# Kernel tuning notes

Measured on AMD Instinct MI355X. Metric: run time of the kernel, lower is better.

## Reference

```python
import jax, jax.numpy as jnp
import numpy as np

STATE_LEN = 128
SEQ_LEN = 2048
NUM_ITERS = 2
DIM_IN = 1024
DIM_H = 64
BATCH = 2
T_TOTAL = SEQ_LEN + 2 * STATE_LEN  # 2304
NEG = -1e30  # large-negative causal mask (avoids -inf NaNs under autodiff)


def _ln(x, g, b):
    m = jnp.mean(x, axis=-1, keepdims=True)
    v = jnp.var(x, axis=-1, keepdims=True)
    return (x - m) / jnp.sqrt(v + 1e-5) * g + b


def setup_inputs() -> dict:
    key = jax.random.key(0)
    ks = jax.random.split(key, 16)

    def w(k, fi, fo):
        # torch nn.Linear-style fan-in scaled init (keeps logits O(1))
        return jax.random.normal(k, (fi, fo), jnp.float32) / np.sqrt(fi)

    return {
        "x": jax.random.normal(ks[0], (BATCH, T_TOTAL, DIM_IN), jnp.float32),
        "Wh": w(ks[1], DIM_IN, DIM_H),
        "Whs": w(ks[2], DIM_IN, DIM_H),
        "Whe": w(ks[3], DIM_IN, DIM_H),
        "Wk": w(ks[4], DIM_H, DIM_H),
        "Wq": w(ks[5], DIM_H, DIM_H),
        "Wv": w(ks[6], DIM_H, DIM_H),
        "Wks": w(ks[7], DIM_H, DIM_H),
        "Wqs": w(ks[8], DIM_H, DIM_H),
        "Wvs": w(ks[9], DIM_H, DIM_H),
        "Wke": w(ks[10], DIM_H, DIM_H),
        "Wqe": w(ks[11], DIM_H, DIM_H),
        "Wve": w(ks[12], DIM_H, DIM_H),
        "ln_g": jnp.ones((DIM_IN,), jnp.float32),
        "ln_b": jnp.zeros((DIM_IN,), jnp.float32),
        "ln_gs": jnp.ones((DIM_IN,), jnp.float32),
        "ln_bs": jnp.zeros((DIM_IN,), jnp.float32),
        "ln_ge": jnp.ones((DIM_IN,), jnp.float32),
        "ln_be": jnp.zeros((DIM_IN,), jnp.float32),
        "cope_emb": jax.random.normal(ks[13], (DIM_H, T_TOTAL), jnp.float32),
    }


def reference(x, Wh, Whs, Whe, Wk, Wq, Wv, Wks, Wqs, Wvs, Wke, Wqe, Wve,
              ln_g, ln_b, ln_gs, ln_bs, ln_ge, ln_be, cope_emb):
    S = STATE_LEN
    # extract_state: [state_start | seq | state_end] along token dim
    xs, xm, xe = x[:, :S], x[:, S:-S], x[:, -S:]
    xm = _ln(xm, ln_g, ln_b)
    xs = _ln(xs, ln_gs, ln_bs)
    xe = _ln(xe, ln_ge, ln_be)

    mem = xm @ Wh                 # (B, L, D)
    mem_s = xs @ Whs              # (B, S, D)
    mem_e = xe @ Whe              # (B, S, D)

    scale = 1.0 / np.sqrt(DIM_H)  # xformers default scale (beta=None)
    tril = jnp.tril(jnp.ones((T_TOTAL, T_TOTAL), bool))
    mask = jnp.where(tril, 0.0, NEG)  # log of lower-triangular ones

    mem_full = None
    for ix in range(NUM_ITERS):
        k = jnp.concatenate([mem_s @ Wks, mem @ Wk, mem_e @ Wke], axis=1)  # (B,T,D)
        q = jnp.concatenate([mem_s @ Wqs, mem @ Wq, mem_e @ Wqe], axis=1)
        v = jnp.concatenate([mem_s @ Wvs, mem @ Wv, mem_e @ Wve], axis=1)

        logits = jnp.einsum('btd,bsd->bts', q, k)  # unscaled, as in CoPE gates
        if ix == 0:
            # CoPE: sigmoid-gated reverse cumsum positions + interpolated embedding bias
            gates = jax.nn.sigmoid(logits)
            pos = jnp.flip(jnp.cumsum(jnp.flip(gates, -1), axis=-1), -1)
            pos = jnp.minimum(pos, float(T_TOTAL - 1))
            pos_floor = jnp.floor(pos)
            pos_ceil = jnp.ceil(pos)
            logits_int = jnp.einsum('btd,dn->btn', q, cope_emb)  # (B,T,T)
            lc = jnp.take_along_axis(logits_int, pos_ceil.astype(jnp.int32), axis=-1)
            lf = jnp.take_along_axis(logits_int, pos_floor.astype(jnp.int32), axis=-1)
            wfrac = pos - pos_floor
            bias = lc * wfrac + lf * (1.0 - wfrac)
            scores = logits * scale + mask + bias
        else:
            scores = logits * scale + mask

        attn = jax.nn.softmax(scores, axis=-1)
        mem_full = jnp.einsum('bts,bsd->btd', attn, v)  # (B,T,D)
        if ix < NUM_ITERS - 1:
            mem_s, mem, mem_e = mem_full[:, :S], mem_full[:, S:-S], mem_full[:, -S:]
    return mem_full
```

## Files before the change

### kernel.cpp

```cpp
#include <hip/hip_runtime.h>

#define T_TOT 2304
#define S_LEN 128
#define D_IN  1024
#define D_H   64
#define BATCH 2
#define NROW  (BATCH * T_TOT)
#define CH    (T_TOT / 256)
#define SCALE 0.125f
#define KCHUNKS 8
#define KCW   (D_IN / KCHUNKS)

typedef unsigned short u16;
typedef __attribute__((ext_vector_type(8))) short short8;
typedef __attribute__((ext_vector_type(4))) float f32x4;
typedef __attribute__((ext_vector_type(4))) unsigned short u16x4;

static __device__ __forceinline__ u16 f2bf(float f) {
    unsigned u = __float_as_uint(f);
    unsigned r = (u + 0x7fffu + ((u >> 16) & 1u)) >> 16;
    return (u16)r;
}
static __device__ __forceinline__ float bf2f(u16 s) {
    return __uint_as_float((unsigned)s << 16);
}

__global__ __launch_bounds__(256) void k_ln(
    const float* __restrict__ x,
    const float* __restrict__ ln_g,  const float* __restrict__ ln_b,
    const float* __restrict__ ln_gs, const float* __restrict__ ln_bs,
    const float* __restrict__ ln_ge, const float* __restrict__ ln_be,
    u16* __restrict__ xn_hi, u16* __restrict__ xn_lo)
{
    __shared__ float red1[256], red2[256];
    const int row = blockIdx.x;
    const int t = row % T_TOT;
    const int tid = threadIdx.x;

    const float *gg, *bb;
    if (t < S_LEN)               { gg = ln_gs; bb = ln_bs; }
    else if (t >= T_TOT - S_LEN) { gg = ln_ge; bb = ln_be; }
    else                         { gg = ln_g;  bb = ln_b;  }

    const float4 xv = *(const float4*)(x + (size_t)row * D_IN + 4 * tid);
    float s  = xv.x + xv.y + xv.z + xv.w;
    float s2 = xv.x * xv.x + xv.y * xv.y + xv.z * xv.z + xv.w * xv.w;
    red1[tid] = s; red2[tid] = s2; __syncthreads();
    for (int off = 128; off > 0; off >>= 1) {
        if (tid < off) { red1[tid] += red1[tid + off]; red2[tid] += red2[tid + off]; }
        __syncthreads();
    }
    const float mean = red1[0] * (1.f / D_IN);
    const float var  = red2[0] * (1.f / D_IN) - mean * mean;
    const float rstd = rsqrtf(var + 1e-5f);

    const float4 gv = *(const float4*)(gg + 4 * tid);
    const float4 bv = *(const float4*)(bb + 4 * tid);
    float o0 = (xv.x - mean) * rstd * gv.x + bv.x;
    float o1 = (xv.y - mean) * rstd * gv.y + bv.y;
    float o2 = (xv.z - mean) * rstd * gv.z + bv.z;
    float o3 = (xv.w - mean) * rstd * gv.w + bv.w;

    u16x4 hv, lv;
    hv[0] = f2bf(o0); lv[0] = f2bf(o0 - bf2f(hv[0]));
    hv[1] = f2bf(o1); lv[1] = f2bf(o1 - bf2f(hv[1]));
    hv[2] = f2bf(o2); lv[2] = f2bf(o2 - bf2f(hv[2]));
    hv[3] = f2bf(o3); lv[3] = f2bf(o3 - bf2f(hv[3]));
    *(u16x4*)(xn_hi + (size_t)row * D_IN + 4 * tid) = hv;
    *(u16x4*)(xn_lo + (size_t)row * D_IN + 4 * tid) = lv;
}

#define WPREP_N (3 * D_H * D_IN)
__global__ __launch_bounds__(256) void k_prep(
    const float* __restrict__ Wh, const float* __restrict__ Whs, const float* __restrict__ Whe,
    const float* __restrict__ cope,
    u16* __restrict__ wT_hi, u16* __restrict__ wT_lo,
    u16* __restrict__ cT_hi, u16* __restrict__ cT_lo)
{
    const int gid = blockIdx.x * 256 + threadIdx.x;
    if (gid < WPREP_N) {
        const int seg = gid >> 16;
        const int o = gid & 65535;
        const int j = o >> 10, k = o & 1023;
        const float* W = seg == 0 ? Wh : (seg == 1 ? Whs : Whe);
        const float f = W[k * D_H + j];
        const u16 hi = f2bf(f);
        wT_hi[gid] = hi;
        wT_lo[gid] = f2bf(f - bf2f(hi));
    } else {
        const int idx = gid - WPREP_N;
        if (idx < T_TOT * D_H) {
            const int n = idx >> 6, d = idx & 63;
            const float f = cope[(size_t)d * T_TOT + n];
            const u16 hi = f2bf(f);
            cT_hi[idx] = hi;
            cT_lo[idx] = f2bf(f - bf2f(hi));
        }
    }
}

__global__ __launch_bounds__(256) void k_hgemm(
    const u16* __restrict__ xn_hi, const u16* __restrict__ xn_lo,
    const u16* __restrict__ wT_hi, const u16* __restrict__ wT_lo,
    float* __restrict__ h_part)
{
    const int tile = blockIdx.x;
    const int kc   = blockIdx.y;
    const int k0   = kc * KCW;
    const int tt = tile % 36;
    const int seg = tt < 2 ? 1 : (tt >= 34 ? 2 : 0);

    __shared__ u16 Bh[64 * KCW];
    __shared__ u16 Bl[64 * KCW];

    const int tid = threadIdx.x;
    {
        const int r = tid >> 2;
        const int c0 = (tid & 3) * 32;
        const u16* sh = wT_hi + ((size_t)seg * D_H + r) * D_IN + k0 + c0;
        const u16* sl = wT_lo + ((size_t)seg * D_H + r) * D_IN + k0 + c0;
        const int sw = (r & 7) << 3;
        #pragma unroll
        for (int u = 0; u < 4; ++u) {
            const int col = c0 + 8 * u;
            *(short8*)&Bh[r * KCW + (col ^ sw)] = *(const short8*)(sh + 8 * u);
            *(short8*)&Bl[r * KCW + (col ^ sw)] = *(const short8*)(sl + 8 * u);
        }
    }
    __syncthreads();

    const int w = tid >> 6;
    const int lane = tid & 63;
    const int l15 = lane & 15, lg4 = lane >> 4;
    const int row0 = tile * 64 + w * 16;

    const size_t abase = (size_t)(row0 + l15) * D_IN + k0 + 8 * lg4;
    f32x4 acc[4] = {};

    #pragma unroll
    for (int kk = 0; kk < KCW / 32; ++kk) {
        short8 ah = *(const short8*)(xn_hi + abase + kk * 32);
        short8 al = *(const short8*)(xn_lo + abase + kk * 32);
        #pragma unroll
        for (int j = 0; j < 4; ++j) {
            const int brow = j * 16 + l15;
            const int col = (kk * 32 + 8 * lg4) ^ ((brow & 7) << 3);
            short8 bh = *(const short8*)&Bh[brow * KCW + col];
            short8 bl = *(const short8*)&Bl[brow * KCW + col];
            acc[j] = __builtin_amdgcn_mfma_f32_16x16x32_bf16(al, bh, acc[j], 0, 0, 0);
            acc[j] = __builtin_amdgcn_mfma_f32_16x16x32_bf16(ah, bl, acc[j], 0, 0, 0);
            acc[j] = __builtin_amdgcn_mfma_f32_16x16x32_bf16(ah, bh, acc[j], 0, 0, 0);
        }
    }
    float* hp = h_part + (size_t)kc * ((size_t)NROW * D_H);
    #pragma unroll
    for (int j = 0; j < 4; ++j)
        #pragma unroll
        for (int r = 0; r < 4; ++r)
            hp[(size_t)(row0 + 4 * lg4 + r) * D_H + j * 16 + l15] = acc[j][r];
}

__global__ __launch_bounds__(256) void k_hred(
    const float* __restrict__ h_part, float* __restrict__ h)
{
    const size_t idx = (size_t)blockIdx.x * 256 + threadIdx.x;
    const size_t N = (size_t)NROW * D_H;
    float s = 0.f;
    #pragma unroll
    for (int kc = 0; kc < KCHUNKS; ++kc) s += h_part[kc * N + idx];
    h[idx] = s;
}

template <bool SPLIT>
__global__ __launch_bounds__(192) void k_qkv(
    const float* __restrict__ hin,
    const float* __restrict__ Wk,  const float* __restrict__ Wq,  const float* __restrict__ Wv,
    const float* __restrict__ Wks, const float* __restrict__ Wqs, const float* __restrict__ Wvs,
    const float* __restrict__ Wke, const float* __restrict__ Wqe, const float* __restrict__ Wve,
    u16* __restrict__ q_hi, u16* __restrict__ q_lo,
    u16* __restrict__ k_hi, u16* __restrict__ k_lo,
    u16* __restrict__ vT)
{
    __shared__ float hr[D_H];
    const int bid = blockIdx.x;
    const int b = bid / T_TOT, t = bid % T_TOT;
    const int tid = threadIdx.x;

    const float* hrow = hin + ((size_t)b * T_TOT + t) * D_H;
    if (tid < D_H) hr[tid] = hrow[tid];
    __syncthreads();

    const int which = tid >> 6, j = tid & 63;
    const float* W;
    if (t < S_LEN)               W = which == 0 ? Wks : (which == 1 ? Wqs : Wvs);
    else if (t >= T_TOT - S_LEN) W = which == 0 ? Wke : (which == 1 ? Wqe : Wve);
    else                         W = which == 0 ? Wk  : (which == 1 ? Wq  : Wv);

    float acc = 0.f;
    #pragma unroll
    for (int d = 0; d < D_H; ++d) acc += hr[d] * W[d * D_H + j];

    const size_t idx = ((size_t)b * T_TOT + t) * D_H + j;
    u16 hi = f2bf(acc);
    if (which == 0) {
        k_hi[idx] = hi;
        if (SPLIT) k_lo[idx] = f2bf(acc - bf2f(hi));
    } else if (which == 1) {
        q_hi[idx] = hi;
        if (SPLIT) q_lo[idx] = f2bf(acc - bf2f(hi));
    } else {
        vT[((size_t)b * D_H + j) * T_TOT + t] = hi;
    }
}

__global__ __launch_bounds__(256) void k_score2(
    const u16* __restrict__ a_hi, const u16* __restrict__ a_lo,
    const u16* __restrict__ k_hi, const u16* __restrict__ k_lo,
    const u16* __restrict__ c_hi, const u16* __restrict__ c_lo,
    float* __restrict__ logits, float* __restrict__ lint)
{
    const int b  = blockIdx.z;
    const int s0 = blockIdx.x * 128;
    const int t0 = blockIdx.y * 64 + (threadIdx.x >> 6) * 16;
    const int lane = threadIdx.x & 63;
    const int l15 = lane & 15, lg4 = lane >> 4;

    const size_t a_off = ((size_t)(b * T_TOT + t0 + l15)) * D_H + 8 * lg4;
    const short8 ah0 = *(const short8*)(a_hi + a_off);
    const short8 ah1 = *(const short8*)(a_hi + a_off + 32);
    const short8 al0 = *(const short8*)(a_lo + a_off);
    const short8 al1 = *(const short8*)(a_lo + a_off + 32);

    const size_t orow_off = ((size_t)(b * T_TOT + t0 + 4 * lg4)) * T_TOT + s0 + l15;

    const u16* bh = k_hi + (size_t)b * (T_TOT * D_H);
    const u16* bl = k_lo + (size_t)b * (T_TOT * D_H);
    float* o = logits + orow_off;
    #pragma unroll
    for (int pass = 0; pass < 2; ++pass) {
        #pragma unroll
        for (int ni = 0; ni < 8; ++ni) {
            const size_t b_off = ((size_t)(s0 + ni * 16 + l15)) * D_H + 8 * lg4;
            short8 bh0 = *(const short8*)(bh + b_off);
            short8 bh1 = *(const short8*)(bh + b_off + 32);
            short8 bl0 = *(const short8*)(bl + b_off);
            short8 bl1 = *(const short8*)(bl + b_off + 32);
            f32x4 acc = {0.f, 0.f, 0.f, 0.f};
            acc = __builtin_amdgcn_mfma_f32_16x16x32_bf16(al0, bh0, acc, 0, 0, 0);
            acc = __builtin_amdgcn_mfma_f32_16x16x32_bf16(al1, bh1, acc, 0, 0, 0);
            acc = __builtin_amdgcn_mfma_f32_16x16x32_bf16(ah0, bl0, acc, 0, 0, 0);
            acc = __builtin_amdgcn_mfma_f32_16x16x32_bf16(ah1, bl1, acc, 0, 0, 0);
            acc = __builtin_amdgcn_mfma_f32_16x16x32_bf16(ah0, bh0, acc, 0, 0, 0);
            acc = __builtin_amdgcn_mfma_f32_16x16x32_bf16(ah1, bh1, acc, 0, 0, 0);
            #pragma unroll
            for (int r = 0; r < 4; ++r)
                o[(size_t)r * T_TOT + ni * 16] = acc[r];
        }
        bh = c_hi; bl = c_lo;
        o = lint + orow_off;
    }
}

__global__ __launch_bounds__(256) void k_score(
    const u16* __restrict__ a_hi, const u16* __restrict__ b_hi,
    float* __restrict__ out)
{
    const int b  = blockIdx.z;
    const int s0 = blockIdx.x * 128;
    if (s0 > blockIdx.y * 64 + 63) return;
    const int t0 = blockIdx.y * 64 + (threadIdx.x >> 6) * 16;
    const int lane = threadIdx.x & 63;
    const int l15 = lane & 15, lg4 = lane >> 4;

    const size_t a_off = ((size_t)(b * T_TOT + t0 + l15)) * D_H + 8 * lg4;
    short8 ah0 = *(const short8*)(a_hi + a_off);
    short8 ah1 = *(const short8*)(a_hi + a_off + 32);

    const u16* bh = b_hi + (size_t)b * (T_TOT * D_H);
    float* orow = out + ((size_t)(b * T_TOT + t0 + 4 * lg4)) * T_TOT + s0 + l15;

    #pragma unroll
    for (int ni = 0; ni < 8; ++ni) {
        const size_t b_off = ((size_t)(s0 + ni * 16 + l15)) * D_H + 8 * lg4;
        short8 bh0 = *(const short8*)(bh + b_off);
        short8 bh1 = *(const short8*)(bh + b_off + 32);
        f32x4 acc = {0.f, 0.f, 0.f, 0.f};
        acc = __builtin_amdgcn_mfma_f32_16x16x32_bf16(ah0, bh0, acc, 0, 0, 0);
        acc = __builtin_amdgcn_mfma_f32_16x16x32_bf16(ah1, bh1, acc, 0, 0, 0);
        #pragma unroll
        for (int r = 0; r < 4; ++r)
            orow[(size_t)r * T_TOT + ni * 16] = acc[r];
    }
}

__global__ __launch_bounds__(256) void k_pv(
    const float* __restrict__ pbuf, const u16* __restrict__ vT,
    float* __restrict__ out)
{
    const int b  = blockIdx.z;
    const int t0 = blockIdx.x * 16;
    const int j0 = (threadIdx.x >> 6) * 16;
    const int lane = threadIdx.x & 63;
    const int l15 = lane & 15, lg4 = lane >> 4;

    const u16* pb = (const u16*)pbuf
        + ((size_t)(b * T_TOT + t0 + l15)) * (2 * (size_t)T_TOT) + 8 * lg4;
    const u16* vb = vT + ((size_t)(b * D_H + j0 + l15)) * T_TOT + 8 * lg4;

    f32x4 a0 = {}, a1 = {}, a2 = {}, a3 = {};
    const int smax = t0 + 16;
    int sc = 0;
    for (; sc + 128 <= smax; sc += 128) {
        short8 p0 = *(const short8*)(pb + sc);
        short8 v0 = *(const short8*)(vb + sc);
        short8 p1 = *(const short8*)(pb + sc + 32);
        short8 v1 = *(const short8*)(vb + sc + 32);
        short8 p2 = *(const short8*)(pb + sc + 64);
        short8 v2 = *(const short8*)(vb + sc + 64);
        short8 p3 = *(const short8*)(pb + sc + 96);
        short8 v3 = *(const short8*)(vb + sc + 96);
        a0 = __builtin_amdgcn_mfma_f32_16x16x32_bf16(p0, v0, a0, 0, 0, 0);
        a1 = __builtin_amdgcn_mfma_f32_16x16x32_bf16(p1, v1, a1, 0, 0, 0);
        a2 = __builtin_amdgcn_mfma_f32_16x16x32_bf16(p2, v2, a2, 0, 0, 0);
        a3 = __builtin_amdgcn_mfma_f32_16x16x32_bf16(p3, v3, a3, 0, 0, 0);
    }
    for (; sc < smax; sc += 32) {
        short8 p0 = *(const short8*)(pb + sc);
        short8 v0 = *(const short8*)(vb + sc);
        a0 = __builtin_amdgcn_mfma_f32_16x16x32_bf16(p0, v0, a0, 0, 0, 0);
    }
    f32x4 acc = (a0 + a1) + (a2 + a3);
    float* obase = out + ((size_t)(b * T_TOT + t0 + 4 * lg4)) * D_H + j0 + l15;
    #pragma unroll
    for (int r = 0; r < 4; ++r) obase[(size_t)r * D_H] = acc[r];
}

template <bool COPE>
__global__ __launch_bounds__(256) void k_erow(
    const float* __restrict__ logits,
    const float* __restrict__ lint,
    float* __restrict__ pbase)
{
    __shared__ float lg[T_TOT];
    __shared__ float extra[COPE ? 2 * T_TOT : 2];
    __shared__ float wtot[4], wmax[4], wsum[4];

    const int row = blockIdx.x;
    const int t = row % T_TOT;
    const int tid = threadIdx.x;
    const int lane = tid & 63, wid = tid >> 6;
    const float* lrow = logits + (size_t)row * T_TOT;

    if (COPE) {
        for (int r = 0; r < CH; ++r) { int s = tid + 256 * r; lg[s] = lrow[s]; }
    } else {
        for (int r = 0; r < CH; ++r) { int s = tid + 256 * r; if (s <= t) lg[s] = lrow[s]; }
    }
    __syncthreads();

    if (COPE) {
        const int base = tid * CH;
        float gv[CH];
        float lsum = 0.f;
        #pragma unroll
        for (int u = 0; u < CH; ++u) {
            float g = 1.f / (1.f + expf(-lg[base + u]));
            gv[u] = g;
            lsum += g;
        }
        float cs = lsum;
        #pragma unroll
        for (int off = 1; off < 64; off <<= 1) {
            float n = __shfl_up(cs, off);
            if (lane >= off) cs += n;
        }
        if (lane == 63) wtot[wid] = cs;
        __syncthreads();
        float pre = 0.f, tot = 0.f;
        #pragma unroll
        for (int w = 0; w < 4; ++w) {
            float vv = wtot[w];
            tot += vv;
            if (w < wid) pre += vv;
        }
        float run = pre + cs - lsum;
        #pragma unroll
        for (int u = 0; u < CH; ++u) {
            float p = fminf(tot - run, (float)(T_TOT - 1));
            extra[base + u] = p;
            run += gv[u];
        }
        const float* lintrow = lint + (size_t)row * T_TOT;
        for (int r = 0; r < CH; ++r) { int s = tid + 256 * r; extra[T_TOT + s] = lintrow[s]; }
        __syncthreads();
    }

    float scv[CH];
    float mx = -3.4e38f;
    #pragma unroll
    for (int r = 0; r < CH; ++r) {
        int sidx = tid + 256 * r;
        float sc = -3.4e38f;
        if (sidx <= t) {
            sc = lg[sidx] * SCALE;
            if (COPE) {
                float p = extra[sidx];
                float pf = floorf(p);
                int fi = (int)pf;
                int ci = (int)ceilf(p);
                float w = p - pf;
                sc += extra[T_TOT + ci] * w + extra[T_TOT + fi] * (1.f - w);
            }
            mx = fmaxf(mx, sc);
        }
        scv[r] = sc;
    }
    #pragma unroll
    for (int off = 32; off > 0; off >>= 1) mx = fmaxf(mx, __shfl_xor(mx, off));
    if (lane == 0) wmax[wid] = mx;
    __syncthreads();
    mx = fmaxf(fmaxf(wmax[0], wmax[1]), fmaxf(wmax[2], wmax[3]));

    float pvv[CH];
    float psum = 0.f;
    #pragma unroll
    for (int r = 0; r < CH; ++r) {
        int sidx = tid + 256 * r;
        float pv = 0.f;
        if (sidx <= t) { pv = expf(scv[r] - mx); psum += pv; }
        pvv[r] = pv;
    }
    #pragma unroll
    for (int off = 32; off > 0; off >>= 1) psum += __shfl_xor(psum, off);
    if (lane == 0) wsum[wid] = psum;
    __syncthreads();
    const float inv = 1.f / (wsum[0] + wsum[1] + wsum[2] + wsum[3]);

    u16* prow = (u16*)(pbase + (size_t)row * T_TOT);
    #pragma unroll
    for (int r = 0; r < CH; ++r) {
        int sidx = tid + 256 * r;
        prow[sidx] = f2bf(pvv[r] * inv);
    }
}

extern "C" void kernel_launch(void* const* d_in, const int* in_sizes, int n_in,
                              void* d_out, int out_size, void* d_ws, size_t ws_size,
                              hipStream_t stream) {
    const float* x    = (const float*)d_in[0];
    const float* Wh   = (const float*)d_in[1];
    const float* Whs  = (const float*)d_in[2];
    const float* Whe  = (const float*)d_in[3];
    const float* Wk   = (const float*)d_in[4];
    const float* Wq   = (const float*)d_in[5];
    const float* Wv   = (const float*)d_in[6];
    const float* Wks  = (const float*)d_in[7];
    const float* Wqs  = (const float*)d_in[8];
    const float* Wvs  = (const float*)d_in[9];
    const float* Wke  = (const float*)d_in[10];
    const float* Wqe  = (const float*)d_in[11];
    const float* Wve  = (const float*)d_in[12];
    const float* ln_g  = (const float*)d_in[13];
    const float* ln_b  = (const float*)d_in[14];
    const float* ln_gs = (const float*)d_in[15];
    const float* ln_bs = (const float*)d_in[16];
    const float* ln_ge = (const float*)d_in[17];
    const float* ln_be = (const float*)d_in[18];
    const float* cope  = (const float*)d_in[19];

    float* out = (float*)d_out;

    const size_t N = (size_t)NROW * D_H;
    char* W = (char*)d_ws;
    u16* xn_hi  = (u16*)W;    W += (size_t)NROW * D_IN * 2;
    u16* xn_lo  = (u16*)W;    W += (size_t)NROW * D_IN * 2;
    u16* wT_hi  = (u16*)W;    W += (size_t)3 * D_H * D_IN * 2;
    u16* wT_lo  = (u16*)W;    W += (size_t)3 * D_H * D_IN * 2;
    float* h    = (float*)W;  W += N * 4;
    u16* q_hi   = (u16*)W;    W += N * 2;
    u16* q_lo   = (u16*)W;    W += N * 2;
    u16* k_hi   = (u16*)W;    W += N * 2;
    u16* k_lo   = (u16*)W;    W += N * 2;
    u16* vT     = (u16*)W;    W += N * 2;
    u16* cT_hi  = (u16*)W;    W += (size_t)T_TOT * D_H * 2;
    u16* cT_lo  = (u16*)W;    W += (size_t)T_TOT * D_H * 2;
    float* logits = (float*)W; W += (size_t)BATCH * T_TOT * T_TOT * 4;
    float* lint   = (float*)W; W += (size_t)BATCH * T_TOT * T_TOT * 4;
    float* mem1   = (float*)W;

    float* h_part = lint;

    const dim3 sg(T_TOT / 128, T_TOT / 64, BATCH);

    k_ln<<<NROW, 256, 0, stream>>>(x, ln_g, ln_b, ln_gs, ln_bs, ln_ge, ln_be,
                                   xn_hi, xn_lo);
    k_prep<<<(WPREP_N + T_TOT * D_H + 255) / 256, 256, 0, stream>>>(
        Wh, Whs, Whe, cope, wT_hi, wT_lo, cT_hi, cT_lo);
    k_hgemm<<<dim3(NROW / 64, KCHUNKS), 256, 0, stream>>>(xn_hi, xn_lo, wT_hi, wT_lo, h_part);
    k_hred<<<(int)(N / 256), 256, 0, stream>>>(h_part, h);

    k_qkv<true><<<NROW, 192, 0, stream>>>(h, Wk, Wq, Wv, Wks, Wqs, Wvs, Wke, Wqe, Wve,
                                          q_hi, q_lo, k_hi, k_lo, vT);
    k_score2<<<sg, 256, 0, stream>>>(q_hi, q_lo, k_hi, k_lo, cT_hi, cT_lo, logits, lint);
    k_erow<true><<<NROW, 256, 0, stream>>>(logits, lint, lint);
    k_pv<<<dim3(T_TOT / 16, 1, BATCH), 256, 0, stream>>>(lint, vT, mem1);

    k_qkv<false><<<NROW, 192, 0, stream>>>(mem1, Wk, Wq, Wv, Wks, Wqs, Wvs, Wke, Wqe, Wve,
                                           q_hi, q_lo, k_hi, k_lo, vT);
    k_score<<<sg, 256, 0, stream>>>(q_hi, k_hi, logits);
    k_erow<false><<<NROW, 256, 0, stream>>>(logits, nullptr, lint);
    k_pv<<<dim3(T_TOT / 16, 1, BATCH), 256, 0, stream>>>(lint, vT, out);
}
```

Baseline: 189.4 us.

## Fuse score, CoPE softmax and PV into a single flash-style attention kernel

Replaces the separate score GEMM, row-softmax/CoPE, and PV kernels with one fused kernel per 16-row query tile. The kernel recomputes QK logits in three passes (gate sums, max, exp+PV) and keeps the interpolated CoPE logits in shared memory. The goal is to stop materializing the two full T×T fp32 logit buffers in global memory and to drop the extra launches. In exchange the QK MFMA work is repeated across passes, and the large shared-memory footprint limits the kernel to one block per CU.

```diff
diff --git a/kernel.cpp b/kernel.cpp
--- a/kernel.cpp
+++ b/kernel.cpp
@@ -6,10 +6,10 @@
 #define D_H   64
 #define BATCH 2
 #define NROW  (BATCH * T_TOT)
-#define CH    (T_TOT / 256)
 #define SCALE 0.125f
 #define KCHUNKS 8
 #define KCW   (D_IN / KCHUNKS)
+#define TB    16
 
 typedef unsigned short u16;
 typedef __attribute__((ext_vector_type(8))) short short8;
@@ -213,38 +213,82 @@
     }
 }
 
-__global__ __launch_bounds__(256) void k_score2(
-    const u16* __restrict__ a_hi, const u16* __restrict__ a_lo,
+template <bool COPE>
+__global__ __launch_bounds__(256, 1) void k_fattn(
+    const u16* __restrict__ q_hi, const u16* __restrict__ q_lo,
     const u16* __restrict__ k_hi, const u16* __restrict__ k_lo,
     const u16* __restrict__ c_hi, const u16* __restrict__ c_lo,
-    float* __restrict__ logits, float* __restrict__ lint)
+    const u16* __restrict__ vT,
+    float* __restrict__ outp)
 {
-    const int b  = blockIdx.z;
-    const int s0 = blockIdx.x * 128;
-    const int t0 = blockIdx.y * 64 + (threadIdx.x >> 6) * 16;
-    const int lane = threadIdx.x & 63;
+    constexpr int LSTRIDE = T_TOT + 4;
+    __shared__ float lint[COPE ? TB * LSTRIDE : 1];
+    __shared__ float csum[4][TB];
+    __shared__ float wmax[4][TB];
+    __shared__ float wden[4][TB];
+    __shared__ float obuf[TB][D_H];
+    __shared__ u16   pstage[4][TB][32];
+
+    const int nblk = T_TOT / TB;
+    const int b  = blockIdx.x / nblk;
+    const int t0 = (blockIdx.x % nblk) * TB;
+    const int tid  = threadIdx.x;
+    const int wid  = tid >> 6;
+    const int lane = tid & 63;
     const int l15 = lane & 15, lg4 = lane >> 4;
 
     const size_t a_off = ((size_t)(b * T_TOT + t0 + l15)) * D_H + 8 * lg4;
-    const short8 ah0 = *(const short8*)(a_hi + a_off);
-    const short8 ah1 = *(const short8*)(a_hi + a_off + 32);
-    const short8 al0 = *(const short8*)(a_lo + a_off);
-    const short8 al1 = *(const short8*)(a_lo + a_off + 32);
-
-    const size_t orow_off = ((size_t)(b * T_TOT + t0 + 4 * lg4)) * T_TOT + s0 + l15;
-
-    const u16* bh = k_hi + (size_t)b * (T_TOT * D_H);
-    const u16* bl = k_lo + (size_t)b * (T_TOT * D_H);
-    float* o = logits + orow_off;
-    #pragma unroll
-    for (int pass = 0; pass < 2; ++pass) {
-        #pragma unroll
-        for (int ni = 0; ni < 8; ++ni) {
-            const size_t b_off = ((size_t)(s0 + ni * 16 + l15)) * D_H + 8 * lg4;
-            short8 bh0 = *(const short8*)(bh + b_off);
-            short8 bh1 = *(const short8*)(bh + b_off + 32);
-            short8 bl0 = *(const short8*)(bl + b_off);
-            short8 bl1 = *(const short8*)(bl + b_off + 32);
+    const short8 ah0 = *(const short8*)(q_hi + a_off);
+    const short8 ah1 = *(const short8*)(q_hi + a_off + 32);
+    short8 al0 = {}, al1 = {};
+    if (COPE) {
+        al0 = *(const short8*)(q_lo + a_off);
+        al1 = *(const short8*)(q_lo + a_off + 32);
+    }
+
+    const u16* kh = k_hi + (size_t)b * (T_TOT * D_H);
+    const u16* kl = k_lo + (size_t)b * (T_TOT * D_H);
+
+    const int s_lo = wid * (T_TOT / 4);
+    const int s_hi = s_lo + (T_TOT / 4);
+    const int t_max = t0 + TB - 1;
+
+    float base[4] = {}, total[4] = {};
+
+    if (COPE) {
+        float chs[4] = {0.f, 0.f, 0.f, 0.f};
+        for (int sb = s_lo; sb < s_hi; sb += 16) {
+            const size_t b_off = ((size_t)(sb + l15)) * D_H + 8 * lg4;
+            short8 bh0 = *(const short8*)(kh + b_off);
+            short8 bh1 = *(const short8*)(kh + b_off + 32);
+            short8 bl0 = *(const short8*)(kl + b_off);
+            short8 bl1 = *(const short8*)(kl + b_off + 32);
+            f32x4 acc = {0.f, 0.f, 0.f, 0.f};
+            acc = __builtin_amdgcn_mfma_f32_16x16x32_bf16(al0, bh0, acc, 0, 0, 0);
+            acc = __builtin_amdgcn_mfma_f32_16x16x32_bf16(al1, bh1, acc, 0, 0, 0);
+            acc = __builtin_amdgcn_mfma_f32_16x16x32_bf16(ah0, bl0, acc, 0, 0, 0);
+            acc = __builtin_amdgcn_mfma_f32_16x16x32_bf16(ah1, bl1, acc, 0, 0, 0);
+            acc = __builtin_amdgcn_mfma_f32_16x16x32_bf16(ah0, bh0, acc, 0, 0, 0);
+            acc = __builtin_amdgcn_mfma_f32_16x16x32_bf16(ah1, bh1, acc, 0, 0, 0);
+            #pragma unroll
+            for (int r = 0; r < 4; ++r) {
+                float g = __fdividef(1.f, 1.f + __expf(-acc[r]));
+                g += __shfl_xor(g, 1); g += __shfl_xor(g, 2);
+                g += __shfl_xor(g, 4); g += __shfl_xor(g, 8);
+                chs[r] += g;
+            }
+        }
+        if (l15 == 0) {
+            #pragma unroll
+            for (int r = 0; r < 4; ++r) csum[wid][4 * lg4 + r] = chs[r];
+        }
+
+        for (int nb = s_lo; nb < s_hi; nb += 16) {
+            const size_t b_off = ((size_t)(nb + l15)) * D_H + 8 * lg4;
+            short8 bh0 = *(const short8*)(c_hi + b_off);
+            short8 bh1 = *(const short8*)(c_hi + b_off + 32);
+            short8 bl0 = *(const short8*)(c_lo + b_off);
+            short8 bl1 = *(const short8*)(c_lo + b_off + 32);
             f32x4 acc = {0.f, 0.f, 0.f, 0.f};
             acc = __builtin_amdgcn_mfma_f32_16x16x32_bf16(al0, bh0, acc, 0, 0, 0);
             acc = __builtin_amdgcn_mfma_f32_16x16x32_bf16(al1, bh1, acc, 0, 0, 0);
@@ -254,193 +298,173 @@
             acc = __builtin_amdgcn_mfma_f32_16x16x32_bf16(ah1, bh1, acc, 0, 0, 0);
             #pragma unroll
             for (int r = 0; r < 4; ++r)
-                o[(size_t)r * T_TOT + ni * 16] = acc[r];
-        }
-        bh = c_hi; bl = c_lo;
-        o = lint + orow_off;
-    }
-}
-
-__global__ __launch_bounds__(256) void k_score(
-    const u16* __restrict__ a_hi, const u16* __restrict__ b_hi,
-    float* __restrict__ out)
-{
-    const int b  = blockIdx.z;
-    const int s0 = blockIdx.x * 128;
-    if (s0 > blockIdx.y * 64 + 63) return;
-    const int t0 = blockIdx.y * 64 + (threadIdx.x >> 6) * 16;
-    const int lane = threadIdx.x & 63;
-    const int l15 = lane & 15, lg4 = lane >> 4;
-
-    const size_t a_off = ((size_t)(b * T_TOT + t0 + l15)) * D_H + 8 * lg4;
-    short8 ah0 = *(const short8*)(a_hi + a_off);
-    short8 ah1 = *(const short8*)(a_hi + a_off + 32);
-
-    const u16* bh = b_hi + (size_t)b * (T_TOT * D_H);
-    float* orow = out + ((size_t)(b * T_TOT + t0 + 4 * lg4)) * T_TOT + s0 + l15;
-
-    #pragma unroll
-    for (int ni = 0; ni < 8; ++ni) {
-        const size_t b_off = ((size_t)(s0 + ni * 16 + l15)) * D_H + 8 * lg4;
-        short8 bh0 = *(const short8*)(bh + b_off);
-        short8 bh1 = *(const short8*)(bh + b_off + 32);
+                lint[(4 * lg4 + r) * LSTRIDE + nb + l15] = acc[r];
+        }
+        __syncthreads();
+
+        #pragma unroll
+        for (int r = 0; r < 4; ++r) {
+            const int tl = 4 * lg4 + r;
+            const float c0 = csum[0][tl], c1 = csum[1][tl];
+            const float c2 = csum[2][tl], c3 = csum[3][tl];
+            total[r] = ((c0 + c1) + c2) + c3;
+            base[r]  = (wid > 0 ? c0 : 0.f) + (wid > 1 ? c1 : 0.f) + (wid > 2 ? c2 : 0.f);
+        }
+    }
+
+    float mx[4] = {-3.0e38f, -3.0e38f, -3.0e38f, -3.0e38f};
+    float pre[4];
+    #pragma unroll
+    for (int r = 0; r < 4; ++r) pre[r] = base[r];
+
+    for (int sb = s_lo; sb < s_hi && sb <= t_max; sb += 16) {
+        const size_t b_off = ((size_t)(sb + l15)) * D_H + 8 * lg4;
+        short8 bh0 = *(const short8*)(kh + b_off);
+        short8 bh1 = *(const short8*)(kh + b_off + 32);
         f32x4 acc = {0.f, 0.f, 0.f, 0.f};
+        if (COPE) {
+            short8 bl0 = *(const short8*)(kl + b_off);
+            short8 bl1 = *(const short8*)(kl + b_off + 32);
+            acc = __builtin_amdgcn_mfma_f32_16x16x32_bf16(al0, bh0, acc, 0, 0, 0);
+            acc = __builtin_amdgcn_mfma_f32_16x16x32_bf16(al1, bh1, acc, 0, 0, 0);
+            acc = __builtin_amdgcn_mfma_f32_16x16x32_bf16(ah0, bl0, acc, 0, 0, 0);
+            acc = __builtin_amdgcn_mfma_f32_16x16x32_bf16(ah1, bl1, acc, 0, 0, 0);
+        }
         acc = __builtin_amdgcn_mfma_f32_16x16x32_bf16(ah0, bh0, acc, 0, 0, 0);
         acc = __builtin_amdgcn_mfma_f32_16x16x32_bf16(ah1, bh1, acc, 0, 0, 0);
         #pragma unroll
-        for (int r = 0; r < 4; ++r)
-            orow[(size_t)r * T_TOT + ni * 16] = acc[r];
-    }
-}
-
-__global__ __launch_bounds__(256) void k_pv(
-    const float* __restrict__ pbuf, const u16* __restrict__ vT,
-    float* __restrict__ out)
-{
-    const int b  = blockIdx.z;
-    const int t0 = blockIdx.x * 16;
-    const int j0 = (threadIdx.x >> 6) * 16;
-    const int lane = threadIdx.x & 63;
-    const int l15 = lane & 15, lg4 = lane >> 4;
-
-    const u16* pb = (const u16*)pbuf
-        + ((size_t)(b * T_TOT + t0 + l15)) * (2 * (size_t)T_TOT) + 8 * lg4;
-    const u16* vb = vT + ((size_t)(b * D_H + j0 + l15)) * T_TOT + 8 * lg4;
-
-    f32x4 a0 = {}, a1 = {}, a2 = {}, a3 = {};
-    const int smax = t0 + 16;
-    int sc = 0;
-    for (; sc + 128 <= smax; sc += 128) {
-        short8 p0 = *(const short8*)(pb + sc);
-        short8 v0 = *(const short8*)(vb + sc);
-        short8 p1 = *(const short8*)(pb + sc + 32);
-        short8 v1 = *(const short8*)(vb + sc + 32);
-        short8 p2 = *(const short8*)(pb + sc + 64);
-        short8 v2 = *(const short8*)(vb + sc + 64);
-        short8 p3 = *(const short8*)(pb + sc + 96);
-        short8 v3 = *(const short8*)(vb + sc + 96);
-        a0 = __builtin_amdgcn_mfma_f32_16x16x32_bf16(p0, v0, a0, 0, 0, 0);
-        a1 = __builtin_amdgcn_mfma_f32_16x16x32_bf16(p1, v1, a1, 0, 0, 0);
-        a2 = __builtin_amdgcn_mfma_f32_16x16x32_bf16(p2, v2, a2, 0, 0, 0);
-        a3 = __builtin_amdgcn_mfma_f32_16x16x32_bf16(p3, v3, a3, 0, 0, 0);
-    }
-    for (; sc < smax; sc += 32) {
-        short8 p0 = *(const short8*)(pb + sc);
-        short8 v0 = *(const short8*)(vb + sc);
-        a0 = __builtin_amdgcn_mfma_f32_16x16x32_bf16(p0, v0, a0, 0, 0, 0);
-    }
-    f32x4 acc = (a0 + a1) + (a2 + a3);
-    float* obase = out + ((size_t)(b * T_TOT + t0 + 4 * lg4)) * D_H + j0 + l15;
-    #pragma unroll
-    for (int r = 0; r < 4; ++r) obase[(size_t)r * D_H] = acc[r];
-}
-
-template <bool COPE>
-__global__ __launch_bounds__(256) void k_erow(
-    const float* __restrict__ logits,
-    const float* __restrict__ lint,
-    float* __restrict__ pbase)
-{
-    __shared__ float lg[T_TOT];
-    __shared__ float extra[COPE ? 2 * T_TOT : 2];
-    __shared__ float wtot[4], wmax[4], wsum[4];
-
-    const int row = blockIdx.x;
-    const int t = row % T_TOT;
-    const int tid = threadIdx.x;
-    const int lane = tid & 63, wid = tid >> 6;
-    const float* lrow = logits + (size_t)row * T_TOT;
-
-    if (COPE) {
-        for (int r = 0; r < CH; ++r) { int s = tid + 256 * r; lg[s] = lrow[s]; }
-    } else {
-        for (int r = 0; r < CH; ++r) { int s = tid + 256 * r; if (s <= t) lg[s] = lrow[s]; }
+        for (int r = 0; r < 4; ++r) {
+            const int tl = 4 * lg4 + r;
+            float sc = acc[r] * SCALE;
+            if (COPE) {
+                float g = __fdividef(1.f, 1.f + __expf(-acc[r]));
+                float cs = g;
+                { float n = __shfl_up(cs, 1, 16); if (l15 >= 1) cs += n; }
+                { float n = __shfl_up(cs, 2, 16); if (l15 >= 2) cs += n; }
+                { float n = __shfl_up(cs, 4, 16); if (l15 >= 4) cs += n; }
+                { float n = __shfl_up(cs, 8, 16); if (l15 >= 8) cs += n; }
+                float tt = __shfl(cs, lane | 15);
+                float pos = total[r] - (pre[r] + cs - g);
+                pos = fminf(fmaxf(pos, 0.f), (float)(T_TOT - 1));
+                float pf = floorf(pos);
+                int fi = (int)pf;
+                int ci = fi < T_TOT - 1 ? fi + 1 : T_TOT - 1;
+                float w = pos - pf;
+                sc += lint[tl * LSTRIDE + ci] * w + lint[tl * LSTRIDE + fi] * (1.f - w);
+                pre[r] += tt;
+            }
+            if (sb + l15 <= t0 + tl) mx[r] = fmaxf(mx[r], sc);
+        }
+    }
+    #pragma unroll
+    for (int r = 0; r < 4; ++r) {
+        mx[r] = fmaxf(mx[r], __shfl_xor(mx[r], 1));
+        mx[r] = fmaxf(mx[r], __shfl_xor(mx[r], 2));
+        mx[r] = fmaxf(mx[r], __shfl_xor(mx[r], 4));
+        mx[r] = fmaxf(mx[r], __shfl_xor(mx[r], 8));
+    }
+    if (l15 == 0) {
+        #pragma unroll
+        for (int r = 0; r < 4; ++r) wmax[wid][4 * lg4 + r] = mx[r];
     }
     __syncthreads();
-
-    if (COPE) {
-        const int base = tid * CH;
-        float gv[CH];
-        float lsum = 0.f;
-        #pragma unroll
-        for (int u = 0; u < CH; ++u) {
-            float g = 1.f / (1.f + expf(-lg[base + u]));
-            gv[u] = g;
-            lsum += g;
-        }
-        float cs = lsum;
-        #pragma unroll
-        for (int off = 1; off < 64; off <<= 1) {
-            float n = __shfl_up(cs, off);
-            if (lane >= off) cs += n;
-        }
-        if (lane == 63) wtot[wid] = cs;
+    float gmx[4];
+    #pragma unroll
+    for (int r = 0; r < 4; ++r) {
+        const int tl = 4 * lg4 + r;
+        gmx[r] = fmaxf(fmaxf(wmax[0][tl], wmax[1][tl]), fmaxf(wmax[2][tl], wmax[3][tl]));
+    }
+
+    f32x4 oacc[4] = {};
+    float den[4] = {0.f, 0.f, 0.f, 0.f};
+    #pragma unroll
+    for (int r = 0; r < 4; ++r) pre[r] = base[r];
+
+    for (int sb0 = s_lo; sb0 < s_hi && sb0 <= t_max; sb0 += 32) {
+        #pragma unroll
+        for (int hh = 0; hh < 2; ++hh) {
+            const int sb = sb0 + 16 * hh;
+            if (sb <= t_max) {
+                const size_t b_off = ((size_t)(sb + l15)) * D_H + 8 * lg4;
+                short8 bh0 = *(const short8*)(kh + b_off);
+                short8 bh1 = *(const short8*)(kh + b_off + 32);
+                f32x4 acc = {0.f, 0.f, 0.f, 0.f};
+                if (COPE) {
+                    short8 bl0 = *(const short8*)(kl + b_off);
+                    short8 bl1 = *(const short8*)(kl + b_off + 32);
+                    acc = __builtin_amdgcn_mfma_f32_16x16x32_bf16(al0, bh0, acc, 0, 0, 0);
+                    acc = __builtin_amdgcn_mfma_f32_16x16x32_bf16(al1, bh1, acc, 0, 0, 0);
+                    acc = __builtin_amdgcn_mfma_f32_16x16x32_bf16(ah0, bl0, acc, 0, 0, 0);
+                    acc = __builtin_amdgcn_mfma_f32_16x16x32_bf16(ah1, bl1, acc, 0, 0, 0);
+                }
+                acc = __builtin_amdgcn_mfma_f32_16x16x32_bf16(ah0, bh0, acc, 0, 0, 0);
+                acc = __builtin_amdgcn_mfma_f32_16x16x32_bf16(ah1, bh1, acc, 0, 0, 0);
+                #pragma unroll
+                for (int r = 0; r < 4; ++r) {
+                    const int tl = 4 * lg4 + r;
+                    float sc = acc[r] * SCALE;
+                    if (COPE) {
+                        float g = __fdividef(1.f, 1.f + __expf(-acc[r]));
+                        float cs = g;
+                        { float n = __shfl_up(cs, 1, 16); if (l15 >= 1) cs += n; }
+                        { float n = __shfl_up(cs, 2, 16); if (l15 >= 2) cs += n; }
+                        { float n = __shfl_up(cs, 4, 16); if (l15 >= 4) cs += n; }
+                        { float n = __shfl_up(cs, 8, 16); if (l15 >= 8) cs += n; }
+                        float tt = __shfl(cs, lane | 15);
+                        float pos = total[r] - (pre[r] + cs - g);
+                        pos = fminf(fmaxf(pos, 0.f), (float)(T_TOT - 1));
+                        float pf = floorf(pos);
+                        int fi = (int)pf;
+                        int ci = fi < T_TOT - 1 ? fi + 1 : T_TOT - 1;
+                        float w = pos - pf;
+                        sc += lint[tl * LSTRIDE + ci] * w + lint[tl * LSTRIDE + fi] * (1.f - w);
+                        pre[r] += tt;
+                    }
+                    const bool valid = (sb + l15) <= (t0 + tl);
+                    float p = valid ? __expf(sc - gmx[r]) : 0.f;
+                    float pr = p;
+                    pr += __shfl_xor(pr, 1); pr += __shfl_xor(pr, 2);
+                    pr += __shfl_xor(pr, 4); pr += __shfl_xor(pr, 8);
+                    den[r] += pr;
+                    pstage[wid][tl][16 * hh + l15] = f2bf(p);
+                }
+            } else {
+                #pragma unroll
+                for (int r = 0; r < 4; ++r)
+                    pstage[wid][4 * lg4 + r][16 * hh + l15] = 0;
+            }
+        }
+        const short8 pa = *(const short8*)&pstage[wid][l15][8 * lg4];
+        #pragma unroll
+        for (int j = 0; j < 4; ++j) {
+            const size_t v_off = ((size_t)(b * D_H + j * 16 + l15)) * T_TOT + sb0 + 8 * lg4;
+            short8 bv = *(const short8*)(vT + v_off);
+            oacc[j] = __builtin_amdgcn_mfma_f32_16x16x32_bf16(pa, bv, oacc[j], 0, 0, 0);
+        }
+    }
+    if (l15 == 0) {
+        #pragma unroll
+        for (int r = 0; r < 4; ++r) wden[wid][4 * lg4 + r] = den[r];
+    }
+
+    __syncthreads();
+    for (int w = 0; w < 4; ++w) {
+        if (wid == w) {
+            #pragma unroll
+            for (int j = 0; j < 4; ++j)
+                #pragma unroll
+                for (int r = 0; r < 4; ++r) {
+                    float* po = &obuf[4 * lg4 + r][j * 16 + l15];
+                    if (w == 0) *po = oacc[j][r];
+                    else        *po += oacc[j][r];
+                }
+        }
         __syncthreads();
-        float pre = 0.f, tot = 0.f;
-        #pragma unroll
-        for (int w = 0; w < 4; ++w) {
-            float vv = wtot[w];
-            tot += vv;
-            if (w < wid) pre += vv;
-        }
-        float run = pre + cs - lsum;
-        #pragma unroll
-        for (int u = 0; u < CH; ++u) {
-            float p = fminf(tot - run, (float)(T_TOT - 1));
-            extra[base + u] = p;
-            run += gv[u];
-        }
-        const float* lintrow = lint + (size_t)row * T_TOT;
-        for (int r = 0; r < CH; ++r) { int s = tid + 256 * r; extra[T_TOT + s] = lintrow[s]; }
-        __syncthreads();
-    }
-
-    float scv[CH];
-    float mx = -3.4e38f;
-    #pragma unroll
-    for (int r = 0; r < CH; ++r) {
-        int sidx = tid + 256 * r;
-        float sc = -3.4e38f;
-        if (sidx <= t) {
-            sc = lg[sidx] * SCALE;
-            if (COPE) {
-                float p = extra[sidx];
-                float pf = floorf(p);
-                int fi = (int)pf;
-                int ci = (int)ceilf(p);
-                float w = p - pf;
-                sc += extra[T_TOT + ci] * w + extra[T_TOT + fi] * (1.f - w);
-            }
-            mx = fmaxf(mx, sc);
-        }
-        scv[r] = sc;
-    }
-    #pragma unroll
-    for (int off = 32; off > 0; off >>= 1) mx = fmaxf(mx, __shfl_xor(mx, off));
-    if (lane == 0) wmax[wid] = mx;
-    __syncthreads();
-    mx = fmaxf(fmaxf(wmax[0], wmax[1]), fmaxf(wmax[2], wmax[3]));
-
-    float pvv[CH];
-    float psum = 0.f;
-    #pragma unroll
-    for (int r = 0; r < CH; ++r) {
-        int sidx = tid + 256 * r;
-        float pv = 0.f;
-        if (sidx <= t) { pv = expf(scv[r] - mx); psum += pv; }
-        pvv[r] = pv;
-    }
-    #pragma unroll
-    for (int off = 32; off > 0; off >>= 1) psum += __shfl_xor(psum, off);
-    if (lane == 0) wsum[wid] = psum;
-    __syncthreads();
-    const float inv = 1.f / (wsum[0] + wsum[1] + wsum[2] + wsum[3]);
-
-    u16* prow = (u16*)(pbase + (size_t)row * T_TOT);
-    #pragma unroll
-    for (int r = 0; r < CH; ++r) {
-        int sidx = tid + 256 * r;
-        prow[sidx] = f2bf(pvv[r] * inv);
+    }
+    for (int e = tid; e < TB * D_H; e += 256) {
+        const int tl = e >> 6, j = e & 63;
+        const float dn = ((wden[0][tl] + wden[1][tl]) + wden[2][tl]) + wden[3][tl];
+        outp[((size_t)(b * T_TOT + t0 + tl)) * D_H + j] = obuf[tl][j] / dn;
     }
 }
 
@@ -484,13 +508,8 @@
     u16* vT     = (u16*)W;    W += N * 2;
     u16* cT_hi  = (u16*)W;    W += (size_t)T_TOT * D_H * 2;
     u16* cT_lo  = (u16*)W;    W += (size_t)T_TOT * D_H * 2;
-    float* logits = (float*)W; W += (size_t)BATCH * T_TOT * T_TOT * 4;
-    float* lint   = (float*)W; W += (size_t)BATCH * T_TOT * T_TOT * 4;
+    float* h_part = (float*)W; W += (size_t)KCHUNKS * N * 4;
     float* mem1   = (float*)W;
-
-    float* h_part = lint;
-
-    const dim3 sg(T_TOT / 128, T_TOT / 64, BATCH);
 
     k_ln<<<NROW, 256, 0, stream>>>(x, ln_g, ln_b, ln_gs, ln_bs, ln_ge, ln_be,
                                    xn_hi, xn_lo);
@@ -501,13 +520,11 @@
 
     k_qkv<true><<<NROW, 192, 0, stream>>>(h, Wk, Wq, Wv, Wks, Wqs, Wvs, Wke, Wqe, Wve,
                                           q_hi, q_lo, k_hi, k_lo, vT);
-    k_score2<<<sg, 256, 0, stream>>>(q_hi, q_lo, k_hi, k_lo, cT_hi, cT_lo, logits, lint);
-    k_erow<true><<<NROW, 256, 0, stream>>>(logits, lint, lint);
-    k_pv<<<dim3(T_TOT / 16, 1, BATCH), 256, 0, stream>>>(lint, vT, mem1);
+    k_fattn<true><<<BATCH * (T_TOT / TB), 256, 0, stream>>>(
+        q_hi, q_lo, k_hi, k_lo, cT_hi, cT_lo, vT, mem1);
 
     k_qkv<false><<<NROW, 192, 0, stream>>>(mem1, Wk, Wq, Wv, Wks, Wqs, Wvs, Wke, Wqe, Wve,
                                            q_hi, q_lo, k_hi, k_lo, vT);
-    k_score<<<sg, 256, 0, stream>>>(q_hi, k_hi, logits);
-    k_erow<false><<<NROW, 256, 0, stream>>>(logits, nullptr, lint);
-    k_pv<<<dim3(T_TOT / 16, 1, BATCH), 256, 0, stream>>>(lint, vT, out);
-}
+    k_fattn<false><<<BATCH * (T_TOT / TB), 256, 0, stream>>>(
+        q_hi, q_hi, k_hi, k_hi, cT_hi, cT_lo, vT, out);
+}
```

Result: slower. 330.6 us (+74.6%).

## Fuse second-iteration attention into flash-style kernel and coalesce score2 stores via LDS

Applied to the files above, without the earlier changes.

Replaces the second iteration's score, softmax-row and PV kernels with one fused kernel. For each 16-row query tile it computes QK^T twice (a max pass, then an exp/accumulate pass) split across four waves by key range, and does the PV MFMA from an LDS-staged bf16 P. This removes the full T×T logits and probability round trips to global memory for iteration two. Separately, score2 now stages its MFMA outputs in shared memory and writes float4 rows for coalesced stores. The trade-offs are recomputing QK^T, only 288 blocks whose causal work is imbalanced, and a per-wave LDS reduction of the output accumulators.

```diff
diff --git a/kernel.cpp b/kernel.cpp
--- a/kernel.cpp
+++ b/kernel.cpp
@@ -10,6 +10,7 @@
 #define SCALE 0.125f
 #define KCHUNKS 8
 #define KCW   (D_IN / KCHUNKS)
+#define TB    16
 
 typedef unsigned short u16;
 typedef __attribute__((ext_vector_type(8))) short short8;
@@ -213,15 +214,19 @@
     }
 }
 
+#define SSTRIDE 132
 __global__ __launch_bounds__(256) void k_score2(
     const u16* __restrict__ a_hi, const u16* __restrict__ a_lo,
     const u16* __restrict__ k_hi, const u16* __restrict__ k_lo,
     const u16* __restrict__ c_hi, const u16* __restrict__ c_lo,
     float* __restrict__ logits, float* __restrict__ lint)
 {
+    __shared__ float stg[64 * SSTRIDE];
+
     const int b  = blockIdx.z;
     const int s0 = blockIdx.x * 128;
-    const int t0 = blockIdx.y * 64 + (threadIdx.x >> 6) * 16;
+    const int wid = threadIdx.x >> 6;
+    const int t0 = blockIdx.y * 64 + wid * 16;
     const int lane = threadIdx.x & 63;
     const int l15 = lane & 15, lg4 = lane >> 4;
 
@@ -231,13 +236,13 @@
     const short8 al0 = *(const short8*)(a_lo + a_off);
     const short8 al1 = *(const short8*)(a_lo + a_off + 32);
 
-    const size_t orow_off = ((size_t)(b * T_TOT + t0 + 4 * lg4)) * T_TOT + s0 + l15;
-
     const u16* bh = k_hi + (size_t)b * (T_TOT * D_H);
     const u16* bl = k_lo + (size_t)b * (T_TOT * D_H);
-    float* o = logits + orow_off;
+    float* o = logits;
+
     #pragma unroll
     for (int pass = 0; pass < 2; ++pass) {
+        f32x4 accs[8];
         #pragma unroll
         for (int ni = 0; ni < 8; ++ni) {
             const size_t b_off = ((size_t)(s0 + ni * 16 + l15)) * D_H + 8 * lg4;
@@ -252,44 +257,26 @@
             acc = __builtin_amdgcn_mfma_f32_16x16x32_bf16(ah1, bl1, acc, 0, 0, 0);
             acc = __builtin_amdgcn_mfma_f32_16x16x32_bf16(ah0, bh0, acc, 0, 0, 0);
             acc = __builtin_amdgcn_mfma_f32_16x16x32_bf16(ah1, bh1, acc, 0, 0, 0);
+            accs[ni] = acc;
+        }
+        #pragma unroll
+        for (int ni = 0; ni < 8; ++ni)
             #pragma unroll
             for (int r = 0; r < 4; ++r)
-                o[(size_t)r * T_TOT + ni * 16] = acc[r];
-        }
+                stg[(wid * 16 + 4 * lg4 + r) * SSTRIDE + ni * 16 + l15] = accs[ni][r];
+        __syncthreads();
+        const int trow = blockIdx.y * 64;
+        #pragma unroll
+        for (int i = 0; i < 8; ++i) {
+            const int idx = i * 256 + threadIdx.x;
+            const int row = idx >> 5;
+            const int c4 = (idx & 31) * 4;
+            *(float4*)&o[((size_t)(b * T_TOT + trow + row)) * T_TOT + s0 + c4] =
+                *(const float4*)&stg[row * SSTRIDE + c4];
+        }
+        __syncthreads();
         bh = c_hi; bl = c_lo;
-        o = lint + orow_off;
-    }
-}
-
-__global__ __launch_bounds__(256) void k_score(
-    const u16* __restrict__ a_hi, const u16* __restrict__ b_hi,
-    float* __restrict__ out)
-{
-    const int b  = blockIdx.z;
-    const int s0 = blockIdx.x * 128;
-    if (s0 > blockIdx.y * 64 + 63) return;
-    const int t0 = blockIdx.y * 64 + (threadIdx.x >> 6) * 16;
-    const int lane = threadIdx.x & 63;
-    const int l15 = lane & 15, lg4 = lane >> 4;
-
-    const size_t a_off = ((size_t)(b * T_TOT + t0 + l15)) * D_H + 8 * lg4;
-    short8 ah0 = *(const short8*)(a_hi + a_off);
-    short8 ah1 = *(const short8*)(a_hi + a_off + 32);
-
-    const u16* bh = b_hi + (size_t)b * (T_TOT * D_H);
-    float* orow = out + ((size_t)(b * T_TOT + t0 + 4 * lg4)) * T_TOT + s0 + l15;
-
-    #pragma unroll
-    for (int ni = 0; ni < 8; ++ni) {
-        const size_t b_off = ((size_t)(s0 + ni * 16 + l15)) * D_H + 8 * lg4;
-        short8 bh0 = *(const short8*)(bh + b_off);
-        short8 bh1 = *(const short8*)(bh + b_off + 32);
-        f32x4 acc = {0.f, 0.f, 0.f, 0.f};
-        acc = __builtin_amdgcn_mfma_f32_16x16x32_bf16(ah0, bh0, acc, 0, 0, 0);
-        acc = __builtin_amdgcn_mfma_f32_16x16x32_bf16(ah1, bh1, acc, 0, 0, 0);
-        #pragma unroll
-        for (int r = 0; r < 4; ++r)
-            orow[(size_t)r * T_TOT + ni * 16] = acc[r];
+        o = lint;
     }
 }
 
@@ -335,14 +322,13 @@
     for (int r = 0; r < 4; ++r) obase[(size_t)r * D_H] = acc[r];
 }
 
-template <bool COPE>
 __global__ __launch_bounds__(256) void k_erow(
     const float* __restrict__ logits,
     const float* __restrict__ lint,
     float* __restrict__ pbase)
 {
     __shared__ float lg[T_TOT];
-    __shared__ float extra[COPE ? 2 * T_TOT : 2];
+    __shared__ float extra[2 * T_TOT];
     __shared__ float wtot[4], wmax[4], wsum[4];
 
     const int row = blockIdx.x;
@@ -351,14 +337,10 @@
     const int lane = tid & 63, wid = tid >> 6;
     const float* lrow = logits + (size_t)row * T_TOT;
 
-    if (COPE) {
-        for (int r = 0; r < CH; ++r) { int s = tid + 256 * r; lg[s] = lrow[s]; }
-    } else {
-        for (int r = 0; r < CH; ++r) { int s = tid + 256 * r; if (s <= t) lg[s] = lrow[s]; }
-    }
+    for (int r = 0; r < CH; ++r) { int s = tid + 256 * r; lg[s] = lrow[s]; }
     __syncthreads();
 
-    if (COPE) {
+    {
         const int base = tid * CH;
         float gv[CH];
         float lsum = 0.f;
@@ -403,14 +385,12 @@
         float sc = -3.4e38f;
         if (sidx <= t) {
             sc = lg[sidx] * SCALE;
-            if (COPE) {
-                float p = extra[sidx];
-                float pf = floorf(p);
-                int fi = (int)pf;
-                int ci = (int)ceilf(p);
-                float w = p - pf;
-                sc += extra[T_TOT + ci] * w + extra[T_TOT + fi] * (1.f - w);
-            }
+            float p = extra[sidx];
+            float pf = floorf(p);
+            int fi = (int)pf;
+            int ci = (int)ceilf(p);
+            float w = p - pf;
+            sc += extra[T_TOT + ci] * w + extra[T_TOT + fi] * (1.f - w);
             mx = fmaxf(mx, sc);
         }
         scv[r] = sc;
@@ -441,6 +421,130 @@
     for (int r = 0; r < CH; ++r) {
         int sidx = tid + 256 * r;
         prow[sidx] = f2bf(pvv[r] * inv);
+    }
+}
+
+__global__ __launch_bounds__(256) void k_fattn1(
+    const u16* __restrict__ q_hi, const u16* __restrict__ k_hi,
+    const u16* __restrict__ vT, float* __restrict__ outp)
+{
+    __shared__ float wmax[4][TB];
+    __shared__ float wden[4][TB];
+    __shared__ float obuf[TB][D_H];
+    __shared__ u16   pstage[4][TB][32];
+
+    const int nblk = T_TOT / TB;
+    const int b  = blockIdx.x / nblk;
+    const int t0 = (blockIdx.x % nblk) * TB;
+    const int tid  = threadIdx.x;
+    const int wid  = tid >> 6;
+    const int lane = tid & 63;
+    const int l15 = lane & 15, lg4 = lane >> 4;
+
+    const size_t a_off = ((size_t)(b * T_TOT + t0 + l15)) * D_H + 8 * lg4;
+    const short8 ah0 = *(const short8*)(q_hi + a_off);
+    const short8 ah1 = *(const short8*)(q_hi + a_off + 32);
+
+    const u16* kh = k_hi + (size_t)b * (T_TOT * D_H);
+
+    const int s_lo = wid * (T_TOT / 4);
+    const int s_hi = s_lo + (T_TOT / 4);
+    const int t_max = t0 + TB - 1;
+
+    float mx[4] = {-3.0e38f, -3.0e38f, -3.0e38f, -3.0e38f};
+    for (int sb = s_lo; sb < s_hi && sb <= t_max; sb += 16) {
+        const size_t b_off = ((size_t)(sb + l15)) * D_H + 8 * lg4;
+        short8 bh0 = *(const short8*)(kh + b_off);
+        short8 bh1 = *(const short8*)(kh + b_off + 32);
+        f32x4 acc = {0.f, 0.f, 0.f, 0.f};
+        acc = __builtin_amdgcn_mfma_f32_16x16x32_bf16(ah0, bh0, acc, 0, 0, 0);
+        acc = __builtin_amdgcn_mfma_f32_16x16x32_bf16(ah1, bh1, acc, 0, 0, 0);
+        #pragma unroll
+        for (int r = 0; r < 4; ++r) {
+            if (sb + l15 <= t0 + 4 * lg4 + r) mx[r] = fmaxf(mx[r], acc[r] * SCALE);
+        }
+    }
+    #pragma unroll
+    for (int r = 0; r < 4; ++r) {
+        mx[r] = fmaxf(mx[r], __shfl_xor(mx[r], 1));
+        mx[r] = fmaxf(mx[r], __shfl_xor(mx[r], 2));
+        mx[r] = fmaxf(mx[r], __shfl_xor(mx[r], 4));
+        mx[r] = fmaxf(mx[r], __shfl_xor(mx[r], 8));
+    }
+    if (l15 == 0) {
+        #pragma unroll
+        for (int r = 0; r < 4; ++r) wmax[wid][4 * lg4 + r] = mx[r];
+    }
+    __syncthreads();
+    float gmx[4];
+    #pragma unroll
+    for (int r = 0; r < 4; ++r) {
+        const int tl = 4 * lg4 + r;
+        gmx[r] = fmaxf(fmaxf(wmax[0][tl], wmax[1][tl]), fmaxf(wmax[2][tl], wmax[3][tl]));
+    }
+
+    f32x4 oacc[4] = {};
+    float den[4] = {0.f, 0.f, 0.f, 0.f};
+
+    for (int sb0 = s_lo; sb0 < s_hi && sb0 <= t_max; sb0 += 32) {
+        #pragma unroll
+        for (int hh = 0; hh < 2; ++hh) {
+            const int sb = sb0 + 16 * hh;
+            if (sb <= t_max) {
+                const size_t b_off = ((size_t)(sb + l15)) * D_H + 8 * lg4;
+                short8 bh0 = *(const short8*)(kh + b_off);
+                short8 bh1 = *(const short8*)(kh + b_off + 32);
+                f32x4 acc = {0.f, 0.f, 0.f, 0.f};
+                acc = __builtin_amdgcn_mfma_f32_16x16x32_bf16(ah0, bh0, acc, 0, 0, 0);
+                acc = __builtin_amdgcn_mfma_f32_16x16x32_bf16(ah1, bh1, acc, 0, 0, 0);
+                #pragma unroll
+                for (int r = 0; r < 4; ++r) {
+                    const int tl = 4 * lg4 + r;
+                    const bool valid = (sb + l15) <= (t0 + tl);
+                    float p = valid ? __expf(acc[r] * SCALE - gmx[r]) : 0.f;
+                    float pr = p;
+                    pr += __shfl_xor(pr, 1); pr += __shfl_xor(pr, 2);
+                    pr += __shfl_xor(pr, 4); pr += __shfl_xor(pr, 8);
+                    den[r] += pr;
+                    pstage[wid][tl][16 * hh + l15] = f2bf(p);
+                }
+            } else {
+                #pragma unroll
+                for (int r = 0; r < 4; ++r)
+                    pstage[wid][4 * lg4 + r][16 * hh + l15] = 0;
+            }
+        }
+        const short8 pa = *(const short8*)&pstage[wid][l15][8 * lg4];
+        #pragma unroll
+        for (int j = 0; j < 4; ++j) {
+            const size_t v_off = ((size_t)(b * D_H + j * 16 + l15)) * T_TOT + sb0 + 8 * lg4;
+            short8 bv = *(const short8*)(vT + v_off);
+            oacc[j] = __builtin_amdgcn_mfma_f32_16x16x32_bf16(pa, bv, oacc[j], 0, 0, 0);
+        }
+    }
+    if (l15 == 0) {
+        #pragma unroll
+        for (int r = 0; r < 4; ++r) wden[wid][4 * lg4 + r] = den[r];
+    }
+
+    __syncthreads();
+    for (int w = 0; w < 4; ++w) {
+        if (wid == w) {
+            #pragma unroll
+            for (int j = 0; j < 4; ++j)
+                #pragma unroll
+                for (int r = 0; r < 4; ++r) {
+                    float* po = &obuf[4 * lg4 + r][j * 16 + l15];
+                    if (w == 0) *po = oacc[j][r];
+                    else        *po += oacc[j][r];
+                }
+        }
+        __syncthreads();
+    }
+    for (int e = tid; e < TB * D_H; e += 256) {
+        const int tl = e >> 6, j = e & 63;
+        const float dn = ((wden[0][tl] + wden[1][tl]) + wden[2][tl]) + wden[3][tl];
+        outp[((size_t)(b * T_TOT + t0 + tl)) * D_H + j] = obuf[tl][j] / dn;
     }
 }
 
@@ -502,12 +606,10 @@
     k_qkv<true><<<NROW, 192, 0, stream>>>(h, Wk, Wq, Wv, Wks, Wqs, Wvs, Wke, Wqe, Wve,
                                           q_hi, q_lo, k_hi, k_lo, vT);
     k_score2<<<sg, 256, 0, stream>>>(q_hi, q_lo, k_hi, k_lo, cT_hi, cT_lo, logits, lint);
-    k_erow<true><<<NROW, 256, 0, stream>>>(logits, lint, lint);
+    k_erow<<<NROW, 256, 0, stream>>>(logits, lint, lint);
     k_pv<<<dim3(T_TOT / 16, 1, BATCH), 256, 0, stream>>>(lint, vT, mem1);
 
     k_qkv<false><<<NROW, 192, 0, stream>>>(mem1, Wk, Wq, Wv, Wks, Wqs, Wvs, Wke, Wqe, Wve,
                                            q_hi, q_lo, k_hi, k_lo, vT);
-    k_score<<<sg, 256, 0, stream>>>(q_hi, k_hi, logits);
-    k_erow<false><<<NROW, 256, 0, stream>>>(logits, nullptr, lint);
-    k_pv<<<dim3(T_TOT / 16, 1, BATCH), 256, 0, stream>>>(lint, vT, out);
-}
+    k_fattn1<<<BATCH * (T_TOT / TB), 256, 0, stream>>>(q_hi, k_hi, vT, out);
+}
```

Measured after the change: 191.3 us. About the same (+1.0%).
